# Kernel optimization log

Hardware: AMD Instinct MI355X
Metric: run time of the kernel (lower is better)

The kernel has to match this reference:

```python
import jax, jax.numpy as jnp
import numpy as np

B, T, H, W_SP, C_IN = 8, 16, 64, 64, 32
F = 64  # output_channels


def _conv(x, w):
    # x: (B,H,W,Cin), w: (kh,kw,Cin,Cout), 'same' padding, stride 1
    return jax.lax.conv_general_dilated(
        x, w, window_strides=(1, 1), padding='SAME',
        dimension_numbers=('NHWC', 'HWIO', 'NHWC'))


def setup_inputs() -> dict:
    key = jax.random.key(0)
    k1, k2, k3 = jax.random.split(key, 3)
    x = jax.random.normal(k1, (B, T, H, W_SP, C_IN), dtype=jnp.float32)
    # Keras ConvLSTM2D kernels: gates stacked [i, f, c, o] along last axis
    W = jax.random.normal(k2, (3, 3, C_IN, 4 * F), dtype=jnp.float32) * 0.05
    U = jax.random.normal(k3, (3, 3, F, 4 * F), dtype=jnp.float32) * 0.05
    b = jnp.zeros((4 * F,), dtype=jnp.float32)
    return {"x": x, "W": W, "U": U, "b": b}


def reference(x, W, U, b):
    # ConvLSTM2D: activation='relu', recurrent_activation='hard_sigmoid',
    # return_sequences=False -> final hidden state (B,H,W,F)
    rec_act = jax.nn.hard_sigmoid  # relu6(x+3)/6
    act = jax.nn.relu

    h0 = jnp.zeros((x.shape[0], x.shape[2], x.shape[3], F), dtype=x.dtype)
    c0 = jnp.zeros_like(h0)

    def step(carry, x_t):
        h, c = carry
        z = _conv(x_t, W) + _conv(h, U) + b  # (B,H,W,4F)
        zi, zf, zc, zo = jnp.split(z, 4, axis=-1)
        i = rec_act(zi)
        f = rec_act(zf)
        o = rec_act(zo)
        c_new = f * c + i * act(zc)
        h_new = o * act(c_new)
        return (h_new, c_new), None

    xs = jnp.transpose(x, (1, 0, 2, 3, 4))  # (T,B,H,W,Cin)
    (h_final, _), _ = jax.lax.scan(step, (h0, c0), xs)
    return h_final
```

## Files before the change

### kernel.cpp

```cpp
#include <hip/hip_runtime.h>


#define TSTEPS 16

typedef short bf16x8 __attribute__((ext_vector_type(8)));
typedef float f32x4 __attribute__((ext_vector_type(4)));
typedef unsigned int __attribute__((address_space(1))) gu32;
typedef unsigned int __attribute__((address_space(3))) lu32;

__device__ __forceinline__ float hsig(float x) {
    return fminf(fmaxf((x + 3.0f) * (1.0f / 6.0f), 0.0f), 1.0f);
}

__device__ __forceinline__ unsigned short f2bf(float f) {
    union { float f; unsigned int u; } v; v.f = f;
    unsigned int r = v.u + 0x7fffu + ((v.u >> 16) & 1u);
    return (unsigned short)(r >> 16);
}

__global__ __launch_bounds__(256)
void prepack_w(const float* __restrict__ Wg, const float* __restrict__ Ug,
               unsigned short* __restrict__ out)
{
    int idx = blockIdx.x * 256 + threadIdx.x;
    if (idx >= 27648) return;
    int lane = idx & 63;
    int nt   = (idx >> 6) & 15;
    int s    = idx >> 10;
    int col = lane & 15, quad = lane >> 4;
    int n = nt * 16 + col;
    int k0 = quad * 8;
    const float* src;
    if (s < 9) {
        src = Wg + ((size_t)s * 32 + k0) * 256 + n;
    } else {
        int ss = s - 9; int tap = ss >> 1; int half = ss & 1;
        src = Ug + ((size_t)tap * 64 + half * 32 + k0) * 256 + n;
    }
    unsigned short tmp[8];
    #pragma unroll
    for (int j = 0; j < 8; ++j) tmp[j] = f2bf(src[(size_t)j * 256]);
    *(uint4*)(out + (size_t)idx * 8) = *(uint4*)tmp;
}

template<int NS>
__global__ __launch_bounds__(512)
__attribute__((amdgpu_waves_per_eu(2, 2)))
void convlstm_step(const float* __restrict__ x,
                   const unsigned short* __restrict__ wpk,
                   const float* __restrict__ bias,
                   const unsigned short* __restrict__ h_in,
                   float* __restrict__ c_st,
                   unsigned short* __restrict__ h_out,
                   int t, int is_last)
{
    constexpr bool HP = (NS == 27);
    constexpr int  P  = 6;

    __shared__ __align__(16) unsigned short xs_s[180 * 40];
    __shared__ __align__(16) unsigned short hs_s[HP ? 180 * 72 : 8];
    __shared__ __align__(16) unsigned short bring[P * 16 * 512];

    const int tid = threadIdx.x;
    const int gx0 = blockIdx.x * 8;
    const int gy0 = blockIdx.y * 16;
    const int b   = blockIdx.z;

    const int lane  = tid & 63;
    const int w     = tid >> 6;
    const int pxgrp = w >> 2;
    const int ngrp  = w & 3;
    const int quad  = lane >> 4;
    const int m     = lane & 15;
    const int ch    = ngrp * 16 + m;

    auto issueDMA = [&](int s) {
        int slot = s % P;
        #pragma unroll
        for (int g = 0; g < 2; ++g) {
            int nt = w + 8 * g;
            const unsigned short* gp = wpk + ((size_t)(s * 16 + nt) * 64 + lane) * 8;
            unsigned short* lp = bring + ((size_t)slot * 16 + nt) * 512;
            __builtin_amdgcn_global_load_lds((const gu32*)gp, (lu32*)lp, 16, 0, 0);
        }
    };

    issueDMA(0);
    issueDMA(1);
    issueDMA(2);

    {
        const float* xt = x + (((size_t)b * TSTEPS + t) * (size_t)(64 * 64 * 32));
        #pragma unroll 3
        for (int idx = tid; idx < 180 * 8; idx += 512) {
            int pix = idx >> 3, q = idx & 7;
            int iy = pix / 10, ix = pix - iy * 10;
            int gy = gy0 + iy - 1, gx = gx0 + ix - 1;
            unsigned short o[4] = {0, 0, 0, 0};
            if ((unsigned)gy < 64u && (unsigned)gx < 64u) {
                float4 v = *(const float4*)(xt + ((size_t)(gy * 64 + gx) * 32) + q * 4);
                o[0] = f2bf(v.x); o[1] = f2bf(v.y); o[2] = f2bf(v.z); o[3] = f2bf(v.w);
            }
            *(ushort4*)(xs_s + pix * 40 + q * 4) = *(ushort4*)o;
        }
    }
    if constexpr (HP) {
        const unsigned short* hb = h_in + ((size_t)b * (64 * 64 * 64));
        #pragma unroll 3
        for (int idx = tid; idx < 180 * 8; idx += 512) {
            int pix = idx >> 3, q = idx & 7;
            int iy = pix / 10, ix = pix - iy * 10;
            int gy = gy0 + iy - 1, gx = gx0 + ix - 1;
            uint4 v = make_uint4(0u, 0u, 0u, 0u);
            if ((unsigned)gy < 64u && (unsigned)gx < 64u)
                v = *(const uint4*)(hb + ((size_t)(gy * 64 + gx) * 64) + q * 8);
            *(uint4*)(hs_s + pix * 72 + q * 8) = v;
        }
    }
    __syncthreads();

    int xb[4], hb_[4];
    #pragma unroll
    for (int mt = 0; mt < 4; ++mt) {
        int p = mt * 16 + m;
        int row = pxgrp * 8 + (p >> 3);
        int cc  = p & 7;
        xb[mt]  = (row * 10 + cc) * 40 + quad * 8;
        hb_[mt] = (row * 10 + cc) * 72 + quad * 8;
    }

    f32x4 acc[4][4];
    #pragma unroll
    for (int g = 0; g < 4; ++g) {
        float bv = bias[g * 64 + ch];
        f32x4 bi = (f32x4){bv, bv, bv, bv};
        #pragma unroll
        for (int mt = 0; mt < 4; ++mt) acc[mt][g] = bi;
    }

    #pragma unroll
    for (int g0 = 0; g0 < NS; g0 += 3) {
        if (g0 + 3 < NS) { issueDMA(g0 + 3); issueDMA(g0 + 4); issueDMA(g0 + 5); }

        #pragma unroll
        for (int j = 0; j < 3; ++j) {
            const int s = g0 + j;
            const int slot = s % P;

            bf16x8 bfr[4];
            #pragma unroll
            for (int g = 0; g < 4; ++g)
                bfr[g] = *(const bf16x8*)(bring + ((size_t)slot * 16 + (ngrp + 4 * g)) * 512 + lane * 8);

            bf16x8 a[4];
            if (s < 9) {
                int taplin = (s / 3) * 10 + (s % 3);
                #pragma unroll
                for (int mt = 0; mt < 4; ++mt)
                    a[mt] = *(const bf16x8*)(xs_s + xb[mt] + taplin * 40);
            } else {
                int ss = s - 9, tap = ss >> 1, half = ss & 1;
                int taplin = (tap / 3) * 10 + (tap % 3);
                #pragma unroll
                for (int mt = 0; mt < 4; ++mt)
                    a[mt] = *(const bf16x8*)(hs_s + hb_[mt] + taplin * 72 + half * 32);
            }

            #pragma unroll
            for (int g = 0; g < 4; ++g)
                #pragma unroll
                for (int mt = 0; mt < 4; ++mt)
                    acc[mt][g] = __builtin_amdgcn_mfma_f32_16x16x32_bf16(a[mt], bfr[g], acc[mt][g], 0, 0, 0);
        }

        __syncthreads();
    }

    #pragma unroll
    for (int mt = 0; mt < 4; ++mt) {
        #pragma unroll
        for (int r = 0; r < 4; ++r) {
            int p = mt * 16 + quad * 4 + r;
            int py = pxgrp * 8 + (p >> 3), px = p & 7;
            size_t gidx = (((size_t)b * 64 + (gy0 + py)) * 64 + (gx0 + px)) * 64 + ch;
            float zi = acc[mt][0][r];
            float zf = acc[mt][1][r];
            float zc = acc[mt][2][r];
            float zo = acc[mt][3][r];
            float c_prev = HP ? c_st[gidx] : 0.0f;
            float cn = hsig(zf) * c_prev + hsig(zi) * fmaxf(zc, 0.0f);
            float hn = hsig(zo) * fmaxf(cn, 0.0f);
            if (is_last) {
                c_st[gidx] = hn;
            } else {
                c_st[gidx] = cn;
                h_out[gidx] = f2bf(hn);
            }
        }
    }
}

extern "C" void kernel_launch(void* const* d_in, const int* in_sizes, int n_in,
                              void* d_out, int out_size, void* d_ws, size_t ws_size,
                              hipStream_t stream) {
    const float* x  = (const float*)d_in[0];
    const float* Wg = (const float*)d_in[1];
    const float* Ug = (const float*)d_in[2];
    const float* bs = (const float*)d_in[3];

    unsigned short* wpk = (unsigned short*)d_ws;
    unsigned short* h0  = (unsigned short*)((char*)d_ws + 27 * 16 * 64 * 8 * 2);
    unsigned short* h1  = h0 + (size_t)8 * 64 * 64 * 64;
    float* cS = (float*)d_out;

    prepack_w<<<108, 256, 0, stream>>>(Wg, Ug, wpk);

    dim3 grid(8, 4, 8);
    dim3 block(512);
    for (int t = 0; t < TSTEPS; ++t) {
        const unsigned short* hin = (t == 0) ? h0 : ((t & 1) ? h0 : h1);
        unsigned short* hout = (t & 1) ? h1 : h0;
        if (t == 0) {
            convlstm_step<9><<<grid, block, 0, stream>>>(x, wpk, bs, hin, cS, hout, t, 0);
        } else {
            convlstm_step<27><<<grid, block, 0, stream>>>(x, wpk, bs, hin, cS, hout,
                                                          t, (t == TSTEPS - 1) ? 1 : 0);
        }
    }
}
```

Baseline: 430.3 us.

## Fuse all timesteps into one persistent cooperative kernel with grid sync

Replaces the 16 per-timestep launches with a single cooperative kernel that loops over time and uses grid.sync between steps. The cell state stays in registers instead of round-tripping through global memory. Each block writes its own new h tile straight into shared memory, so only the halo ring has to be reloaded from global. This removes launch gaps and global traffic, at the cost of grid-wide barriers and a requirement that all 256 blocks be co-resident.

```diff
diff --git a/kernel.cpp b/kernel.cpp
--- a/kernel.cpp
+++ b/kernel.cpp
@@ -1,4 +1,7 @@
 #include <hip/hip_runtime.h>
+#include <hip/hip_cooperative_groups.h>
+
+namespace cg = cooperative_groups;
 
 
 #define TSTEPS 16
@@ -43,23 +46,22 @@
     *(uint4*)(out + (size_t)idx * 8) = *(uint4*)tmp;
 }
 
-template<int NS>
 __global__ __launch_bounds__(512)
 __attribute__((amdgpu_waves_per_eu(2, 2)))
-void convlstm_step(const float* __restrict__ x,
-                   const unsigned short* __restrict__ wpk,
-                   const float* __restrict__ bias,
-                   const unsigned short* __restrict__ h_in,
-                   float* __restrict__ c_st,
-                   unsigned short* __restrict__ h_out,
-                   int t, int is_last)
+void convlstm_all(const float* __restrict__ x,
+                  const unsigned short* __restrict__ wpk,
+                  const float* __restrict__ bias,
+                  float* __restrict__ c_st,
+                  unsigned short* __restrict__ hA,
+                  unsigned short* __restrict__ hB)
 {
-    constexpr bool HP = (NS == 27);
-    constexpr int  P  = 6;
+    constexpr int P = 6;
 
     __shared__ __align__(16) unsigned short xs_s[180 * 40];
-    __shared__ __align__(16) unsigned short hs_s[HP ? 180 * 72 : 8];
+    __shared__ __align__(16) unsigned short hs_s[180 * 72];
     __shared__ __align__(16) unsigned short bring[P * 16 * 512];
+
+    cg::grid_group grid = cg::this_grid();
 
     const int tid = threadIdx.x;
     const int gx0 = blockIdx.x * 8;
@@ -85,40 +87,6 @@
         }
     };
 
-    issueDMA(0);
-    issueDMA(1);
-    issueDMA(2);
-
-    {
-        const float* xt = x + (((size_t)b * TSTEPS + t) * (size_t)(64 * 64 * 32));
-        #pragma unroll 3
-        for (int idx = tid; idx < 180 * 8; idx += 512) {
-            int pix = idx >> 3, q = idx & 7;
-            int iy = pix / 10, ix = pix - iy * 10;
-            int gy = gy0 + iy - 1, gx = gx0 + ix - 1;
-            unsigned short o[4] = {0, 0, 0, 0};
-            if ((unsigned)gy < 64u && (unsigned)gx < 64u) {
-                float4 v = *(const float4*)(xt + ((size_t)(gy * 64 + gx) * 32) + q * 4);
-                o[0] = f2bf(v.x); o[1] = f2bf(v.y); o[2] = f2bf(v.z); o[3] = f2bf(v.w);
-            }
-            *(ushort4*)(xs_s + pix * 40 + q * 4) = *(ushort4*)o;
-        }
-    }
-    if constexpr (HP) {
-        const unsigned short* hb = h_in + ((size_t)b * (64 * 64 * 64));
-        #pragma unroll 3
-        for (int idx = tid; idx < 180 * 8; idx += 512) {
-            int pix = idx >> 3, q = idx & 7;
-            int iy = pix / 10, ix = pix - iy * 10;
-            int gy = gy0 + iy - 1, gx = gx0 + ix - 1;
-            uint4 v = make_uint4(0u, 0u, 0u, 0u);
-            if ((unsigned)gy < 64u && (unsigned)gx < 64u)
-                v = *(const uint4*)(hb + ((size_t)(gy * 64 + gx) * 64) + q * 8);
-            *(uint4*)(hs_s + pix * 72 + q * 8) = v;
-        }
-    }
-    __syncthreads();
-
     int xb[4], hb_[4];
     #pragma unroll
     for (int mt = 0; mt < 4; ++mt) {
@@ -128,76 +96,144 @@
         xb[mt]  = (row * 10 + cc) * 40 + quad * 8;
         hb_[mt] = (row * 10 + cc) * 72 + quad * 8;
     }
-
-    f32x4 acc[4][4];
-    #pragma unroll
-    for (int g = 0; g < 4; ++g) {
-        float bv = bias[g * 64 + ch];
-        f32x4 bi = (f32x4){bv, bv, bv, bv};
-        #pragma unroll
-        for (int mt = 0; mt < 4; ++mt) acc[mt][g] = bi;
-    }
-
-    #pragma unroll
-    for (int g0 = 0; g0 < NS; g0 += 3) {
-        if (g0 + 3 < NS) { issueDMA(g0 + 3); issueDMA(g0 + 4); issueDMA(g0 + 5); }
-
-        #pragma unroll
-        for (int j = 0; j < 3; ++j) {
-            const int s = g0 + j;
-            const int slot = s % P;
-
-            bf16x8 bfr[4];
+    float bv[4];
+    #pragma unroll
+    for (int g = 0; g < 4; ++g) bv[g] = bias[g * 64 + ch];
+
+    float creg[4][4];
+    #pragma unroll
+    for (int mt = 0; mt < 4; ++mt)
+        #pragma unroll
+        for (int r = 0; r < 4; ++r) creg[mt][r] = 0.0f;
+
+    const unsigned short* hin = hA;
+    unsigned short*       hout = hB;
+
+#define KGROUP(G0, DOISSUE)                                                      \
+    {                                                                            \
+        if (DOISSUE) { issueDMA((G0) + 3); issueDMA((G0) + 4); issueDMA((G0) + 5); } \
+        _Pragma("unroll")                                                        \
+        for (int j = 0; j < 3; ++j) {                                            \
+            const int s = (G0) + j;                                              \
+            const int slot = s % P;                                              \
+            bf16x8 bfr[4];                                                       \
+            _Pragma("unroll")                                                    \
+            for (int g = 0; g < 4; ++g)                                          \
+                bfr[g] = *(const bf16x8*)(bring + ((size_t)slot * 16 + (ngrp + 4 * g)) * 512 + lane * 8); \
+            bf16x8 a[4];                                                         \
+            if (s < 9) {                                                         \
+                int taplin = (s / 3) * 10 + (s % 3);                             \
+                _Pragma("unroll")                                                \
+                for (int mt = 0; mt < 4; ++mt)                                   \
+                    a[mt] = *(const bf16x8*)(xs_s + xb[mt] + taplin * 40);       \
+            } else {                                                             \
+                int ss = s - 9, tap = ss >> 1, half = ss & 1;                    \
+                int taplin = (tap / 3) * 10 + (tap % 3);                         \
+                _Pragma("unroll")                                                \
+                for (int mt = 0; mt < 4; ++mt)                                   \
+                    a[mt] = *(const bf16x8*)(hs_s + hb_[mt] + taplin * 72 + half * 32); \
+            }                                                                    \
+            _Pragma("unroll")                                                    \
+            for (int g = 0; g < 4; ++g) {                                        \
+                _Pragma("unroll")                                                \
+                for (int mt = 0; mt < 4; ++mt)                                   \
+                    acc[mt][g] = __builtin_amdgcn_mfma_f32_16x16x32_bf16(a[mt], bfr[g], acc[mt][g], 0, 0, 0); \
+            }                                                                    \
+        }                                                                        \
+        __syncthreads();                                                         \
+    }
+
+    #pragma unroll 1
+    for (int t = 0; t < TSTEPS; ++t) {
+        const bool hp = (t > 0);
+
+        issueDMA(0); issueDMA(1); issueDMA(2);
+
+        {
+            const float* xt = x + (((size_t)b * TSTEPS + t) * (size_t)(64 * 64 * 32));
+            #pragma unroll 3
+            for (int idx = tid; idx < 180 * 8; idx += 512) {
+                int pix = idx >> 3, q = idx & 7;
+                int iy = pix / 10, ix = pix - iy * 10;
+                int gy = gy0 + iy - 1, gx = gx0 + ix - 1;
+                unsigned short o[4] = {0, 0, 0, 0};
+                if ((unsigned)gy < 64u && (unsigned)gx < 64u) {
+                    float4 v = *(const float4*)(xt + ((size_t)(gy * 64 + gx) * 32) + q * 4);
+                    o[0] = f2bf(v.x); o[1] = f2bf(v.y); o[2] = f2bf(v.z); o[3] = f2bf(v.w);
+                }
+                *(ushort4*)(xs_s + pix * 40 + q * 4) = *(ushort4*)o;
+            }
+        }
+        if (hp) {
+            const unsigned short* hb = hin + ((size_t)b * (64 * 64 * 64));
+            for (int idx = tid; idx < 52 * 8; idx += 512) {
+                int pi = idx >> 3, q = idx & 7;
+                int iy, ix;
+                if (pi < 10)      { iy = 0;  ix = pi; }
+                else if (pi < 20) { iy = 17; ix = pi - 10; }
+                else { int j = pi - 20; iy = 1 + (j >> 1); ix = (j & 1) * 9; }
+                int gy = gy0 + iy - 1, gx = gx0 + ix - 1;
+                uint4 v = make_uint4(0u, 0u, 0u, 0u);
+                if ((unsigned)gy < 64u && (unsigned)gx < 64u)
+                    v = *(const uint4*)(hb + ((size_t)(gy * 64 + gx) * 64) + q * 8);
+                *(uint4*)(hs_s + (iy * 10 + ix) * 72 + q * 8) = v;
+            }
+        }
+        __syncthreads();
+
+        f32x4 acc[4][4];
+        #pragma unroll
+        for (int g = 0; g < 4; ++g) {
+            f32x4 bi = (f32x4){bv[g], bv[g], bv[g], bv[g]};
             #pragma unroll
-            for (int g = 0; g < 4; ++g)
-                bfr[g] = *(const bf16x8*)(bring + ((size_t)slot * 16 + (ngrp + 4 * g)) * 512 + lane * 8);
-
-            bf16x8 a[4];
-            if (s < 9) {
-                int taplin = (s / 3) * 10 + (s % 3);
-                #pragma unroll
-                for (int mt = 0; mt < 4; ++mt)
-                    a[mt] = *(const bf16x8*)(xs_s + xb[mt] + taplin * 40);
-            } else {
-                int ss = s - 9, tap = ss >> 1, half = ss & 1;
-                int taplin = (tap / 3) * 10 + (tap % 3);
-                #pragma unroll
-                for (int mt = 0; mt < 4; ++mt)
-                    a[mt] = *(const bf16x8*)(hs_s + hb_[mt] + taplin * 72 + half * 32);
+            for (int mt = 0; mt < 4; ++mt) acc[mt][g] = bi;
+        }
+
+        KGROUP(0, true);
+        KGROUP(3, true);
+        KGROUP(6, hp);
+        if (hp) {
+            KGROUP(9,  true);
+            KGROUP(12, true);
+            KGROUP(15, true);
+            KGROUP(18, true);
+            KGROUP(21, true);
+            KGROUP(24, false);
+        }
+
+        const int last = (t == TSTEPS - 1);
+        #pragma unroll
+        for (int mt = 0; mt < 4; ++mt) {
+            #pragma unroll
+            for (int r = 0; r < 4; ++r) {
+                int p = mt * 16 + quad * 4 + r;
+                int py = pxgrp * 8 + (p >> 3), px = p & 7;
+                size_t gidx = (((size_t)b * 64 + (gy0 + py)) * 64 + (gx0 + px)) * 64 + ch;
+                float zi = acc[mt][0][r];
+                float zf = acc[mt][1][r];
+                float zc = acc[mt][2][r];
+                float zo = acc[mt][3][r];
+                float cn = hsig(zf) * creg[mt][r] + hsig(zi) * fmaxf(zc, 0.0f);
+                float hn = hsig(zo) * fmaxf(cn, 0.0f);
+                creg[mt][r] = cn;
+                if (last) {
+                    c_st[gidx] = hn;
+                } else {
+                    unsigned short hv = f2bf(hn);
+                    hout[gidx] = hv;
+                    hs_s[((py + 1) * 10 + (px + 1)) * 72 + ch] = hv;
+                }
             }
-
-            #pragma unroll
-            for (int g = 0; g < 4; ++g)
-                #pragma unroll
-                for (int mt = 0; mt < 4; ++mt)
-                    acc[mt][g] = __builtin_amdgcn_mfma_f32_16x16x32_bf16(a[mt], bfr[g], acc[mt][g], 0, 0, 0);
-        }
-
-        __syncthreads();
-    }
-
-    #pragma unroll
-    for (int mt = 0; mt < 4; ++mt) {
-        #pragma unroll
-        for (int r = 0; r < 4; ++r) {
-            int p = mt * 16 + quad * 4 + r;
-            int py = pxgrp * 8 + (p >> 3), px = p & 7;
-            size_t gidx = (((size_t)b * 64 + (gy0 + py)) * 64 + (gx0 + px)) * 64 + ch;
-            float zi = acc[mt][0][r];
-            float zf = acc[mt][1][r];
-            float zc = acc[mt][2][r];
-            float zo = acc[mt][3][r];
-            float c_prev = HP ? c_st[gidx] : 0.0f;
-            float cn = hsig(zf) * c_prev + hsig(zi) * fmaxf(zc, 0.0f);
-            float hn = hsig(zo) * fmaxf(cn, 0.0f);
-            if (is_last) {
-                c_st[gidx] = hn;
-            } else {
-                c_st[gidx] = cn;
-                h_out[gidx] = f2bf(hn);
-            }
-        }
-    }
+        }
+
+        if (!last) {
+            __threadfence();
+            grid.sync();
+            const unsigned short* tmp = hin;
+            hin = hout; hout = (unsigned short*)tmp;
+        }
+    }
+#undef KGROUP
 }
 
 extern "C" void kernel_launch(void* const* d_in, const int* in_sizes, int n_in,
@@ -217,14 +253,7 @@
 
     dim3 grid(8, 4, 8);
     dim3 block(512);
-    for (int t = 0; t < TSTEPS; ++t) {
-        const unsigned short* hin = (t == 0) ? h0 : ((t & 1) ? h0 : h1);
-        unsigned short* hout = (t & 1) ? h1 : h0;
-        if (t == 0) {
-            convlstm_step<9><<<grid, block, 0, stream>>>(x, wpk, bs, hin, cS, hout, t, 0);
-        } else {
-            convlstm_step<27><<<grid, block, 0, stream>>>(x, wpk, bs, hin, cS, hout,
-                                                          t, (t == TSTEPS - 1) ? 1 : 0);
-        }
-    }
-}
+    void* args[] = { (void*)&x, (void*)&wpk, (void*)&bs,
+                     (void*)&cS, (void*)&h0, (void*)&h1 };
+    hipLaunchCooperativeKernel((const void*)convlstm_all, grid, block, args, 0, stream);
+}
```

Measured after the change: 1.682 ms. 291% more time.
